# Performance work log

Hardware: AMD Instinct MI355X
Metric: run time of the kernel (lower is better)

The kernel has to match this reference:

```python
import jax, jax.numpy as jnp
import numpy as np

N_NODES = 100000
N_EDGES = 1600000
N_GRAPHS = 2048
F_IN = 33
D = 256


def _graph_conv(x, edge_index, w_rel, b_rel, w_root):
    # PyG GraphConv (aggr='add'): out = lin_rel(sum_j x_j) + lin_root(x)
    src, dst = edge_index[0], edge_index[1]
    agg = jax.ops.segment_sum(x[src], dst, num_segments=x.shape[0])  # [N, F]
    return agg @ w_rel + b_rel + x @ w_root


def setup_inputs() -> dict:
    key = jax.random.key(0)
    ks = jax.random.split(key, 16)
    scale_in = 1.0 / np.sqrt(F_IN)
    scale_d = 1.0 / np.sqrt(D)
    inp = {
        "x": jax.random.normal(ks[0], (N_NODES, F_IN), dtype=jnp.float32),
        "edge_index": jax.random.randint(ks[1], (2, N_EDGES), 0, N_NODES),
        "batch_index": jnp.sort(jax.random.randint(ks[2], (N_NODES,), 0, N_GRAPHS)),
        # initial_conv: GraphConv(F_IN -> D)
        "w_rel0": jax.random.normal(ks[3], (F_IN, D), dtype=jnp.float32) * scale_in,
        "b_rel0": jnp.zeros((D,), dtype=jnp.float32),
        "w_root0": jax.random.normal(ks[4], (F_IN, D), dtype=jnp.float32) * scale_in,
        # conv1..conv3: GraphConv(D -> D)
        "w_rel1": jax.random.normal(ks[5], (D, D), dtype=jnp.float32) * scale_d,
        "b_rel1": jnp.zeros((D,), dtype=jnp.float32),
        "w_root1": jax.random.normal(ks[6], (D, D), dtype=jnp.float32) * scale_d,
        "w_rel2": jax.random.normal(ks[7], (D, D), dtype=jnp.float32) * scale_d,
        "b_rel2": jnp.zeros((D,), dtype=jnp.float32),
        "w_root2": jax.random.normal(ks[8], (D, D), dtype=jnp.float32) * scale_d,
        "w_rel3": jax.random.normal(ks[9], (D, D), dtype=jnp.float32) * scale_d,
        "b_rel3": jnp.zeros((D,), dtype=jnp.float32),
        "w_root3": jax.random.normal(ks[10], (D, D), dtype=jnp.float32) * scale_d,
        # output head Linear(D -> 1)
        "w_out": jax.random.normal(ks[11], (D, 1), dtype=jnp.float32) * scale_d,
        "b_out": jnp.zeros((1,), dtype=jnp.float32),
    }
    return inp


def reference(x, edge_index, batch_index,
              w_rel0, b_rel0, w_root0,
              w_rel1, b_rel1, w_root1,
              w_rel2, b_rel2, w_root2,
              w_rel3, b_rel3, w_root3,
              w_out, b_out):
    # dropout omitted (eval mode)
    h = jax.nn.gelu(_graph_conv(x, edge_index, w_rel0, b_rel0, w_root0))
    h = jax.nn.gelu(_graph_conv(h, edge_index, w_rel1, b_rel1, w_root1))
    h = jax.nn.gelu(_graph_conv(h, edge_index, w_rel2, b_rel2, w_root2))
    h = jax.nn.gelu(_graph_conv(h, edge_index, w_rel3, b_rel3, w_root3))
    # global mean pool over graphs
    sums = jax.ops.segment_sum(h, batch_index, num_segments=N_GRAPHS)          # [G, D]
    counts = jax.ops.segment_sum(jnp.ones((h.shape[0],), h.dtype), batch_index,
                                 num_segments=N_GRAPHS)                         # [G]
    pooled = sums / jnp.maximum(counts, 1.0)[:, None]
    return pooled @ w_out + b_out                                               # [G, 1]
```

## Files before the change

### kernel.cpp

```cpp
#include <hip/hip_runtime.h>
#include <math.h>

#define NN 100000
#define NE 1600000
#define NG 2048
#define FIN 33
#define DD 256

#define SH 8
#define NB ((NN + 255) >> 8)
#define CH 4096
#define PCAP 4608
#define ESCAP 6144

#define RBLKS ((NN + 255) / 256)

typedef __attribute__((ext_vector_type(8))) short bf16x8;
typedef __attribute__((ext_vector_type(4))) float f32x4;

__device__ __forceinline__ float b2f(unsigned short u){
    union { unsigned int i; float f; } c; c.i = ((unsigned int)u) << 16; return c.f;
}
__device__ __forceinline__ unsigned short f2b(float f){
    union { float f; unsigned int u; } c; c.f = f;
    unsigned int r = c.u + 0x7fffu + ((c.u >> 16) & 1u);
    return (unsigned short)(r >> 16);
}

__device__ __forceinline__ float gelu_tanh(float x){
    float z = 0.7978845608028654f * (x + 0.044715f * x * x * x);
    return x / (1.0f + __expf(-2.0f * z));
}

__global__ __launch_bounds__(256) void k_bin(const int* __restrict__ src,
                                             const int* __restrict__ dst,
                                             int* __restrict__ gcur,
                                             int* __restrict__ pairs){
    __shared__ int cnt[NB];
    __shared__ int lb[NB];
    __shared__ int gbase[NB];
    __shared__ int sc[512];
    __shared__ int2 stage[CH];

    int t = threadIdx.x;
    for(int i = t; i < NB; i += 256) cnt[i] = 0;
    __syncthreads();

    int e0 = blockIdx.x * CH;
    int n = NE - e0; if(n > CH) n = CH;

    int  myb[16];
    int  myr[16];
    int2 myp[16];
    #pragma unroll
    for(int k = 0; k < 16; k++){
        int e = e0 + t + k * 256;
        if(e < NE){
            int s = src[e], d = dst[e];
            int b = d >> SH;
            myr[k] = atomicAdd(&cnt[b], 1);
            myb[k] = b;
            myp[k] = make_int2(s, d);
        } else myb[k] = -1;
    }
    __syncthreads();

    sc[t]       = (t       < NB) ? cnt[t]       : 0;
    sc[t + 256] = (t + 256 < NB) ? cnt[t + 256] : 0;
    __syncthreads();
    for(int off = 1; off < 512; off <<= 1){
        int a  = (t >= off)       ? sc[t - off]       : 0;
        int b2 = (t + 256 >= off) ? sc[t + 256 - off] : 0;
        __syncthreads();
        sc[t] += a; sc[t + 256] += b2;
        __syncthreads();
    }
    for(int i = t; i < NB; i += 256){
        lb[i] = sc[i] - cnt[i];
        int c = cnt[i];
        gbase[i] = (c > 0) ? atomicAdd(&gcur[i], c) : 0;
    }
    __syncthreads();

    #pragma unroll
    for(int k = 0; k < 16; k++){
        if(myb[k] >= 0) stage[lb[myb[k]] + myr[k]] = myp[k];
    }
    __syncthreads();

    for(int i = t; i < n; i += 256){
        int2 p = stage[i];
        int b = p.y >> SH;
        int tgt = gbase[b] + (i - lb[b]);
        if(tgt < PCAP) pairs[(size_t)b * PCAP + tgt] = p.x | ((p.y & 255) << 17);
    }
}

__global__ void k_sscan(const int* __restrict__ gcur, int* __restrict__ boff){
    __shared__ int s[512];
    int t = threadIdx.x;
    int v = 0;
    if(t < NB){ v = gcur[t]; if(v > PCAP) v = PCAP; }
    s[t] = v; __syncthreads();
    for(int off = 1; off < 512; off <<= 1){
        int u = (t >= off) ? s[t - off] : 0;
        __syncthreads();
        s[t] += u;
        __syncthreads();
    }
    if(t < NB) boff[t] = s[t] - v;
}

__global__ __launch_bounds__(256) void k_bcsr(const int* __restrict__ pairs,
                                              const int* __restrict__ gcur,
                                              const int* __restrict__ boff,
                                              int* __restrict__ deg,
                                              int* __restrict__ rs,
                                              int* __restrict__ esrc){
    __shared__ int hist[256];
    __shared__ int sc[256];
    __shared__ int cur2[256];
    __shared__ int est[ESCAP];

    int b = blockIdx.x;
    int t = threadIdx.x;
    int m = gcur[b]; if(m > PCAP) m = PCAP;
    int pstart = boff[b];
    const int* bp = pairs + (size_t)b * PCAP;

    hist[t] = 0;
    __syncthreads();
    for(int i = t; i < m; i += 256) atomicAdd(&hist[(bp[i] >> 17) & 255], 1);
    __syncthreads();

    sc[t] = hist[t]; __syncthreads();
    for(int off = 1; off < 256; off <<= 1){
        int u = (t >= off) ? sc[t - off] : 0;
        __syncthreads();
        sc[t] += u;
        __syncthreads();
    }
    int excl = sc[t] - hist[t];
    cur2[t] = excl;
    int node = (b << 8) + t;
    if(node < NN){
        deg[node] = hist[t];
        rs[node]  = pstart + excl;
    }
    __syncthreads();

    for(int i = t; i < m; i += 256){
        int p = bp[i];
        int pos = atomicAdd(&cur2[(p >> 17) & 255], 1);
        int s = p & 0x1FFFF;
        if(pos < ESCAP) est[pos] = s;
        else esrc[pstart + pos] = s;
    }
    __syncthreads();
    int lim = (m < ESCAP) ? m : ESCAP;
    for(int i = t; i < lim; i += 256) esrc[pstart + i] = est[i];
}

__global__ void k_xpad(const float* __restrict__ x, unsigned short* __restrict__ xb){
    int idx = blockIdx.x * 256 + threadIdx.x;
    if(idx >= NN * 64) return;
    int n = idx >> 6, c = idx & 63;
    xb[idx] = (c < FIN) ? f2b(x[(size_t)n * FIN + c]) : 0;
}

__global__ void k_aggx(const unsigned short* __restrict__ xb, const int* __restrict__ rs,
                       const int* __restrict__ deg, const int* __restrict__ esrc,
                       unsigned short* __restrict__ axb){
    int wv = (blockIdx.x * blockDim.x + threadIdx.x) >> 6;
    int lane = threadIdx.x & 63;
    int node = wv * 4 + (lane >> 4);
    int l16 = lane & 15;
    if(node >= NN) return;
    int start = rs[node], cnt = deg[node];
    float a0 = 0.f, a1 = 0.f, a2 = 0.f, a3 = 0.f;
    const unsigned short* xp = xb + l16 * 4;
    int j = 0;
    for(; j + 4 <= cnt; j += 4){
        int e0 = esrc[start+j], e1 = esrc[start+j+1], e2 = esrc[start+j+2], e3 = esrc[start+j+3];
        ushort4 v0 = *(const ushort4*)(xp + (size_t)e0 * 64);
        ushort4 v1 = *(const ushort4*)(xp + (size_t)e1 * 64);
        ushort4 v2 = *(const ushort4*)(xp + (size_t)e2 * 64);
        ushort4 v3 = *(const ushort4*)(xp + (size_t)e3 * 64);
        a0 += (b2f(v0.x) + b2f(v1.x)) + (b2f(v2.x) + b2f(v3.x));
        a1 += (b2f(v0.y) + b2f(v1.y)) + (b2f(v2.y) + b2f(v3.y));
        a2 += (b2f(v0.z) + b2f(v1.z)) + (b2f(v2.z) + b2f(v3.z));
        a3 += (b2f(v0.w) + b2f(v1.w)) + (b2f(v2.w) + b2f(v3.w));
    }
    for(; j < cnt; j++){
        int e = esrc[start + j];
        ushort4 v = *(const ushort4*)(xp + (size_t)e * 64);
        a0 += b2f(v.x); a1 += b2f(v.y); a2 += b2f(v.z); a3 += b2f(v.w);
    }
    ushort4 o; o.x = f2b(a0); o.y = f2b(a1); o.z = f2b(a2); o.w = f2b(a3);
    *(ushort4*)(axb + (size_t)node * 64 + l16 * 4) = o;
}

__global__ void k_agg256(const unsigned short* __restrict__ h, const int* __restrict__ rs,
                         const int* __restrict__ deg, const int* __restrict__ esrc,
                         unsigned short* __restrict__ agg){
    int wv = (blockIdx.x * blockDim.x + threadIdx.x) >> 6;
    int lane = threadIdx.x & 63;
    int node = wv * 2 + (lane >> 5);
    int l32 = lane & 31;
    if(node >= NN) return;
    int start = rs[node], cnt = deg[node];
    float a[8] = {0.f,0.f,0.f,0.f,0.f,0.f,0.f,0.f};
    const unsigned short* hp = h + l32 * 8;
    int j = 0;
    for(; j + 8 <= cnt; j += 8){
        bf16x8 v[8];
        #pragma unroll
        for(int q = 0; q < 8; q++){
            int e = esrc[start + j + q];
            v[q] = *(const bf16x8*)(hp + (size_t)e * DD);
        }
        #pragma unroll
        for(int q = 0; q < 8; q++)
            #pragma unroll
            for(int d = 0; d < 8; d++)
                a[d] += b2f((unsigned short)v[q][d]);
    }
    for(; j < cnt; j++){
        int e = esrc[start + j];
        bf16x8 v = *(const bf16x8*)(hp + (size_t)e * DD);
        #pragma unroll
        for(int d = 0; d < 8; d++) a[d] += b2f((unsigned short)v[d]);
    }
    bf16x8 o;
    #pragma unroll
    for(int d = 0; d < 8; d++) o[d] = (short)f2b(a[d]);
    *(bf16x8*)(agg + (size_t)node * DD + l32 * 8) = o;
}

struct WPtrs { const float* w[6]; };

__global__ void k_wt6(WPtrs wp, unsigned short* __restrict__ btAll){
    __shared__ float s[16][17];
    const float* W = wp.w[blockIdx.z];
    unsigned short* Bt = btAll + (size_t)blockIdx.z * DD * DD;
    int tx = threadIdx.x, ty = threadIdx.y;
    int k = blockIdx.y * 16 + ty;
    int j = blockIdx.x * 16 + tx;
    s[ty][tx] = W[k * DD + j];
    __syncthreads();
    Bt[(size_t)(blockIdx.x * 16 + ty) * DD + blockIdx.y * 16 + tx] = f2b(s[tx][ty]);
}

struct W2Ptrs { const float* w[2]; };

__global__ void k_wt0(W2Ptrs wp, unsigned short* __restrict__ btAll){
    int idx = blockIdx.x * 256 + threadIdx.x;
    if(idx >= DD * 64) return;
    const float* W = wp.w[blockIdx.z];
    unsigned short* Bt = btAll + (size_t)blockIdx.z * DD * 64;
    int j = idx >> 6, k = idx & 63;
    Bt[idx] = (k < FIN) ? f2b(W[(size_t)k * DD + j]) : 0;
}

__global__ void k_cnt(const int* __restrict__ batch, int* __restrict__ gcnt){
    int i = blockIdx.x * 256 + threadIdx.x;
    if(i < NN) atomicAdd(&gcnt[batch[i]], 1);
}

template<int KS, int AST, bool POOL>
__global__ __launch_bounds__(512, 4) void k_mfma_gemm(
    const unsigned short* __restrict__ A0, const unsigned short* __restrict__ A1,
    const unsigned short* __restrict__ Bt0, const unsigned short* __restrict__ Bt1,
    const float* __restrict__ bias, unsigned short* __restrict__ out,
    const int* __restrict__ batch, const float* __restrict__ wout,
    float* __restrict__ gsum)
{
    constexpr int CK  = KS * 32;
    constexpr int BST = CK + 8;
    constexpr int SEG = CK / 8;
    __shared__ unsigned short Bs[128 * BST];

    int t = threadIdx.x;
    int lane = t & 63;
    int w = t >> 6;
    int r16 = lane & 15;
    int kg  = lane >> 4;

    int bid = blockIdx.x;
    int rblk = (bid >> 4) * 8 + (bid & 7);
    int chalf = (bid >> 3) & 1;
    if(rblk >= RBLKS) return;
    int i0 = rblk * 256;
    int jbase = chalf * 128;
    int baseRow = i0 + w * 32;

    f32x4 acc[2][8];
    #pragma unroll
    for(int m = 0; m < 2; m++)
        #pragma unroll
        for(int n = 0; n < 8; n++)
            acc[m][n] = (f32x4){0.f, 0.f, 0.f, 0.f};

    auto loadA = [&](int gks, bf16x8* af){
        const unsigned short* Ap = (gks < KS) ? A0 : A1;
        int kk = ((gks < KS) ? gks : gks - KS) * 32 + kg * 8;
        #pragma unroll
        for(int m = 0; m < 2; m++){
            int gi = baseRow + m * 16 + r16;
            if(gi > NN - 1) gi = NN - 1;
            af[m] = *(const bf16x8*)(Ap + (size_t)gi * AST + kk);
        }
    };

    bf16x8 afb[2][2];
    loadA(0, afb[0]);
    loadA(1, afb[1]);

    #pragma unroll
    for(int c = 0; c < 2; c++){
        const unsigned short* Bp = c ? Bt1 : Bt0;
        if(c) __syncthreads();
        #pragma unroll
        for(int p = 0; p < (128 * SEG) / 512; p++){
            int idx = p * 512 + t;
            int row = idx / SEG;
            int k8 = (idx % SEG) * 8;
            *(bf16x8*)(&Bs[row * BST + k8]) =
                *(const bf16x8*)(Bp + (size_t)(jbase + row) * AST + k8);
        }
        __syncthreads();
        #pragma unroll
        for(int ksl = 0; ksl < KS; ksl++){
            int gks = c * KS + ksl;
            #pragma unroll
            for(int n = 0; n < 8; n++){
                bf16x8 bfr = *(const bf16x8*)(&Bs[(n * 16 + r16) * BST + ksl * 32 + kg * 8]);
                acc[0][n] = __builtin_amdgcn_mfma_f32_16x16x32_bf16(afb[gks & 1][0], bfr, acc[0][n], 0, 0, 0);
                acc[1][n] = __builtin_amdgcn_mfma_f32_16x16x32_bf16(afb[gks & 1][1], bfr, acc[1][n], 0, 0, 0);
            }
            if(gks + 2 < 2 * KS) loadA(gks + 2, afb[gks & 1]);
        }
    }

    int rg = kg * 4;
    if constexpr (!POOL){
        #pragma unroll
        for(int n = 0; n < 8; n++){
            int gj = jbase + n * 16 + r16;
            float bb = bias[gj];
            #pragma unroll
            for(int m = 0; m < 2; m++){
                #pragma unroll
                for(int r = 0; r < 4; r++){
                    int gi = baseRow + m * 16 + rg + r;
                    if(gi < NN)
                        out[(size_t)gi * DD + gj] = f2b(gelu_tanh(acc[m][n][r] + bb));
                }
            }
        }
    } else {
        #pragma unroll
        for(int m = 0; m < 2; m++){
            #pragma unroll
            for(int r = 0; r < 4; r++){
                float s = 0.f;
                #pragma unroll
                for(int n = 0; n < 8; n++){
                    int gj = jbase + n * 16 + r16;
                    s += gelu_tanh(acc[m][n][r] + bias[gj]) * wout[gj];
                }
                s += __shfl_xor(s, 1);
                s += __shfl_xor(s, 2);
                s += __shfl_xor(s, 4);
                s += __shfl_xor(s, 8);
                int gi = baseRow + m * 16 + rg + r;
                if(r16 == 0 && gi < NN)
                    atomicAdd(&gsum[batch[gi]], s);
            }
        }
    }
}

__global__ void k_final(const float* __restrict__ gsum, const int* __restrict__ gcnt,
                        const float* __restrict__ bout, float* __restrict__ out){
    int g = blockIdx.x * 256 + threadIdx.x;
    if(g < NG) out[g] = gsum[g] / fmaxf((float)gcnt[g], 1.f) + bout[0];
}

extern "C" void kernel_launch(void* const* d_in, const int* in_sizes, int n_in,
                              void* d_out, int out_size, void* d_ws, size_t ws_size,
                              hipStream_t stream){
    const float* x       = (const float*)d_in[0];
    const int*   ei      = (const int*)d_in[1];
    const int*   src     = ei;
    const int*   dst     = ei + NE;
    const int*   batch   = (const int*)d_in[2];
    const float* w_rel0  = (const float*)d_in[3];
    const float* b_rel0  = (const float*)d_in[4];
    const float* w_root0 = (const float*)d_in[5];
    const float* w_rel1  = (const float*)d_in[6];
    const float* b_rel1  = (const float*)d_in[7];
    const float* w_root1 = (const float*)d_in[8];
    const float* w_rel2  = (const float*)d_in[9];
    const float* b_rel2  = (const float*)d_in[10];
    const float* w_root2 = (const float*)d_in[11];
    const float* w_rel3  = (const float*)d_in[12];
    const float* b_rel3  = (const float*)d_in[13];
    const float* w_root3 = (const float*)d_in[14];
    const float* w_out   = (const float*)d_in[15];
    const float* b_out   = (const float*)d_in[16];
    float* out = (float*)d_out;

    char* ws = (char*)d_ws;
    size_t off = 0;
    auto alloc = [&](size_t bytes) -> void* {
        void* p = ws + off;
        off = (off + bytes + 255) & ~(size_t)255;
        return p;
    };
    unsigned short* hA  = (unsigned short*)alloc((size_t)NN * DD * 2);
    unsigned short* hB  = (unsigned short*)alloc((size_t)NN * DD * 2);
    unsigned short* agg = (unsigned short*)alloc((size_t)NN * DD * 2);
    int*   deg  = (int*)alloc((size_t)NN * 4);
    int*   rs   = (int*)alloc((size_t)NN * 4);
    int*   esrc = (int*)alloc((size_t)NE * 4);
    int*   gcur = (int*)alloc(512 * 4);
    int*   boff = (int*)alloc(512 * 4);
    float* gsum = (float*)alloc((size_t)NG * 4);
    int*   gcnt = (int*)alloc((size_t)NG * 4);
    unsigned short* btAll = (unsigned short*)alloc((size_t)6 * DD * DD * 2);
    unsigned short* bt0All = (unsigned short*)alloc((size_t)2 * DD * 64 * 2);
    (void)ws_size; (void)in_sizes; (void)n_in; (void)out_size;

    int* pairs = (int*)hB;
    unsigned short* xb  = agg;
    unsigned short* axb = agg + (size_t)NN * 64 + 128;

    hipMemsetAsync(gcur, 0, 512 * 4, stream);
    k_bin<<<(NE + CH - 1) / CH, 256, 0, stream>>>(src, dst, gcur, pairs);
    k_sscan<<<1, 512, 0, stream>>>(gcur, boff);
    k_bcsr<<<NB, 256, 0, stream>>>(pairs, gcur, boff, deg, rs, esrc);

    size_t poolBytes = (size_t)((char*)(gcnt + NG) - (char*)gsum);
    hipMemsetAsync(gsum, 0, poolBytes, stream);
    k_cnt<<<(NN + 255) / 256, 256, 0, stream>>>(batch, gcnt);

    WPtrs wp; wp.w[0] = w_rel1; wp.w[1] = w_root1; wp.w[2] = w_rel2;
    wp.w[3] = w_root2; wp.w[4] = w_rel3; wp.w[5] = w_root3;
    k_wt6<<<dim3(16, 16, 6), dim3(16, 16), 0, stream>>>(wp, btAll);
    W2Ptrs w2; w2.w[0] = w_rel0; w2.w[1] = w_root0;
    k_wt0<<<dim3((DD * 64 + 255) / 256, 1, 2), 256, 0, stream>>>(w2, bt0All);
    k_xpad<<<(NN * 64 + 255) / 256, 256, 0, stream>>>(x, xb);

    unsigned short* bt[6];
    for(int i = 0; i < 6; i++) bt[i] = btAll + (size_t)i * DD * DD;
    unsigned short* bt0r = bt0All;
    unsigned short* bt0o = bt0All + (size_t)DD * 64;

    int agg2Grid = (NN * 32 + 255) / 256;
    int gemmGrid = ((RBLKS + 7) / 8) * 16;

    k_aggx<<<(NN + 15) / 16, 256, 0, stream>>>(xb, rs, deg, esrc, axb);
    k_mfma_gemm<2, 64, false><<<gemmGrid, 512, 0, stream>>>(axb, xb, bt0r, bt0o, b_rel0, hA,
                                                            batch, w_out, gsum);
    k_agg256<<<agg2Grid, 256, 0, stream>>>(hA, rs, deg, esrc, agg);
    k_mfma_gemm<8, 256, false><<<gemmGrid, 512, 0, stream>>>(agg, hA, bt[0], bt[1], b_rel1, hB,
                                                             batch, w_out, gsum);
    k_agg256<<<agg2Grid, 256, 0, stream>>>(hB, rs, deg, esrc, agg);
    k_mfma_gemm<8, 256, false><<<gemmGrid, 512, 0, stream>>>(agg, hB, bt[2], bt[3], b_rel2, hA,
                                                             batch, w_out, gsum);
    k_agg256<<<agg2Grid, 256, 0, stream>>>(hA, rs, deg, esrc, agg);
    k_mfma_gemm<8, 256, true><<<gemmGrid, 512, 0, stream>>>(agg, hA, bt[4], bt[5], b_rel3, hB,
                                                            batch, w_out, gsum);

    k_final<<<(NG + 255) / 256, 256, 0, stream>>>(gsum, gcnt, b_out, out);
}
```

Baseline: 739.7 us.

## Pre-swizzle weights into MFMA fragment layout and drop LDS staging in GEMM

Adds a k_bfrag pre-pass that rearranges the transposed bf16 weights into per-lane MFMA fragment order. The GEMM then reads B fragments straight from global memory (expected to hit L2) with coalesced 16-byte loads, so the LDS tile and its __syncthreads barriers are gone. Blocks shrink to 256 threads and 128 rows, which doubles the grid. The A prefetch double-buffering is also removed, so A loads are no longer overlapped with MFMA and global-memory latency is exposed on every k-step.

```diff
diff --git a/kernel.cpp b/kernel.cpp
--- a/kernel.cpp
+++ b/kernel.cpp
@@ -13,7 +13,7 @@
 #define PCAP 4608
 #define ESCAP 6144
 
-#define RBLKS ((NN + 255) / 256)
+#define RB128 ((NN + 127) / 128)
 
 typedef __attribute__((ext_vector_type(8))) short bf16x8;
 typedef __attribute__((ext_vector_type(4))) float f32x4;
@@ -262,24 +262,34 @@
     Bt[idx] = (k < FIN) ? f2b(W[(size_t)k * DD + j]) : 0;
 }
 
+__global__ void k_bfrag(const unsigned short* __restrict__ btBase,
+                        unsigned short* __restrict__ bfBase,
+                        int ast, int nslots, int inStride, int outStride){
+    int slot = blockIdx.x * 256 + threadIdx.x;
+    if(slot >= nslots) return;
+    const unsigned short* Bt = btBase + (size_t)blockIdx.z * inStride;
+    unsigned short* bf = bfBase + (size_t)blockIdx.z * outStride;
+    int ks = slot >> 10;
+    int rem = slot & 1023;
+    int n = rem >> 6;
+    int l = rem & 63;
+    bf16x8 v = *(const bf16x8*)(Bt + (size_t)(n * 16 + (l & 15)) * ast + ks * 32 + (l >> 4) * 8);
+    *(bf16x8*)(bf + (size_t)slot * 8) = v;
+}
+
 __global__ void k_cnt(const int* __restrict__ batch, int* __restrict__ gcnt){
     int i = blockIdx.x * 256 + threadIdx.x;
     if(i < NN) atomicAdd(&gcnt[batch[i]], 1);
 }
 
 template<int KS, int AST, bool POOL>
-__global__ __launch_bounds__(512, 4) void k_mfma_gemm(
+__global__ __launch_bounds__(256, 4) void k_gemm_nl(
     const unsigned short* __restrict__ A0, const unsigned short* __restrict__ A1,
-    const unsigned short* __restrict__ Bt0, const unsigned short* __restrict__ Bt1,
+    const unsigned short* __restrict__ bp0, const unsigned short* __restrict__ bp1,
     const float* __restrict__ bias, unsigned short* __restrict__ out,
     const int* __restrict__ batch, const float* __restrict__ wout,
     float* __restrict__ gsum)
 {
-    constexpr int CK  = KS * 32;
-    constexpr int BST = CK + 8;
-    constexpr int SEG = CK / 8;
-    __shared__ unsigned short Bs[128 * BST];
-
     int t = threadIdx.x;
     int lane = t & 63;
     int w = t >> 6;
@@ -289,8 +299,8 @@
     int bid = blockIdx.x;
     int rblk = (bid >> 4) * 8 + (bid & 7);
     int chalf = (bid >> 3) & 1;
-    if(rblk >= RBLKS) return;
-    int i0 = rblk * 256;
+    if(rblk >= RB128) return;
+    int i0 = rblk * 128;
     int jbase = chalf * 128;
     int baseRow = i0 + w * 32;
 
@@ -301,44 +311,27 @@
         for(int n = 0; n < 8; n++)
             acc[m][n] = (f32x4){0.f, 0.f, 0.f, 0.f};
 
-    auto loadA = [&](int gks, bf16x8* af){
-        const unsigned short* Ap = (gks < KS) ? A0 : A1;
-        int kk = ((gks < KS) ? gks : gks - KS) * 32 + kg * 8;
-        #pragma unroll
-        for(int m = 0; m < 2; m++){
-            int gi = baseRow + m * 16 + r16;
-            if(gi > NN - 1) gi = NN - 1;
-            af[m] = *(const bf16x8*)(Ap + (size_t)gi * AST + kk);
-        }
-    };
-
-    bf16x8 afb[2][2];
-    loadA(0, afb[0]);
-    loadA(1, afb[1]);
-
     #pragma unroll
     for(int c = 0; c < 2; c++){
-        const unsigned short* Bp = c ? Bt1 : Bt0;
-        if(c) __syncthreads();
-        #pragma unroll
-        for(int p = 0; p < (128 * SEG) / 512; p++){
-            int idx = p * 512 + t;
-            int row = idx / SEG;
-            int k8 = (idx % SEG) * 8;
-            *(bf16x8*)(&Bs[row * BST + k8]) =
-                *(const bf16x8*)(Bp + (size_t)(jbase + row) * AST + k8);
-        }
-        __syncthreads();
+        const unsigned short* Ap = c ? A1 : A0;
+        const unsigned short* Bp = c ? bp1 : bp0;
         #pragma unroll
         for(int ksl = 0; ksl < KS; ksl++){
-            int gks = c * KS + ksl;
+            int kk = ksl * 32 + kg * 8;
+            bf16x8 af[2];
+            #pragma unroll
+            for(int m = 0; m < 2; m++){
+                int gi = baseRow + m * 16 + r16;
+                if(gi > NN - 1) gi = NN - 1;
+                af[m] = *(const bf16x8*)(Ap + (size_t)gi * AST + kk);
+            }
+            const unsigned short* bpp = Bp + (size_t)((ksl * 16 + chalf * 8) * 64 + lane) * 8;
             #pragma unroll
             for(int n = 0; n < 8; n++){
-                bf16x8 bfr = *(const bf16x8*)(&Bs[(n * 16 + r16) * BST + ksl * 32 + kg * 8]);
-                acc[0][n] = __builtin_amdgcn_mfma_f32_16x16x32_bf16(afb[gks & 1][0], bfr, acc[0][n], 0, 0, 0);
-                acc[1][n] = __builtin_amdgcn_mfma_f32_16x16x32_bf16(afb[gks & 1][1], bfr, acc[1][n], 0, 0, 0);
+                bf16x8 bfr = *(const bf16x8*)(bpp + (size_t)n * 64 * 8);
+                acc[0][n] = __builtin_amdgcn_mfma_f32_16x16x32_bf16(af[0], bfr, acc[0][n], 0, 0, 0);
+                acc[1][n] = __builtin_amdgcn_mfma_f32_16x16x32_bf16(af[1], bfr, acc[1][n], 0, 0, 0);
             }
-            if(gks + 2 < 2 * KS) loadA(gks + 2, afb[gks & 1]);
         }
     }
 
@@ -428,8 +421,10 @@
     int*   boff = (int*)alloc(512 * 4);
     float* gsum = (float*)alloc((size_t)NG * 4);
     int*   gcnt = (int*)alloc((size_t)NG * 4);
-    unsigned short* btAll = (unsigned short*)alloc((size_t)6 * DD * DD * 2);
+    unsigned short* btAll  = (unsigned short*)alloc((size_t)6 * DD * DD * 2);
     unsigned short* bt0All = (unsigned short*)alloc((size_t)2 * DD * 64 * 2);
+    unsigned short* bfAll  = (unsigned short*)alloc((size_t)6 * DD * DD * 2);
+    unsigned short* bf0All = (unsigned short*)alloc((size_t)2 * DD * 64 * 2);
     (void)ws_size; (void)in_sizes; (void)n_in; (void)out_size;
 
     int* pairs = (int*)hB;
@@ -452,26 +447,29 @@
     k_wt0<<<dim3((DD * 64 + 255) / 256, 1, 2), 256, 0, stream>>>(w2, bt0All);
     k_xpad<<<(NN * 64 + 255) / 256, 256, 0, stream>>>(x, xb);
 
-    unsigned short* bt[6];
-    for(int i = 0; i < 6; i++) bt[i] = btAll + (size_t)i * DD * DD;
-    unsigned short* bt0r = bt0All;
-    unsigned short* bt0o = bt0All + (size_t)DD * 64;
+    k_bfrag<<<dim3(8192 / 256, 1, 6), 256, 0, stream>>>(btAll, bfAll, DD, 8192, DD * DD, DD * DD);
+    k_bfrag<<<dim3(2048 / 256, 1, 2), 256, 0, stream>>>(bt0All, bf0All, 64, 2048, DD * 64, DD * 64);
+
+    unsigned short* bf[6];
+    for(int i = 0; i < 6; i++) bf[i] = bfAll + (size_t)i * DD * DD;
+    unsigned short* bf0r = bf0All;
+    unsigned short* bf0o = bf0All + (size_t)DD * 64;
 
     int agg2Grid = (NN * 32 + 255) / 256;
-    int gemmGrid = ((RBLKS + 7) / 8) * 16;
+    int gemmGrid = ((RB128 + 7) / 8) * 16;
 
     k_aggx<<<(NN + 15) / 16, 256, 0, stream>>>(xb, rs, deg, esrc, axb);
-    k_mfma_gemm<2, 64, false><<<gemmGrid, 512, 0, stream>>>(axb, xb, bt0r, bt0o, b_rel0, hA,
-                                                            batch, w_out, gsum);
+    k_gemm_nl<2, 64, false><<<gemmGrid, 256, 0, stream>>>(axb, xb, bf0r, bf0o, b_rel0, hA,
+                                                          batch, w_out, gsum);
     k_agg256<<<agg2Grid, 256, 0, stream>>>(hA, rs, deg, esrc, agg);
-    k_mfma_gemm<8, 256, false><<<gemmGrid, 512, 0, stream>>>(agg, hA, bt[0], bt[1], b_rel1, hB,
-                                                             batch, w_out, gsum);
+    k_gemm_nl<8, 256, false><<<gemmGrid, 256, 0, stream>>>(agg, hA, bf[0], bf[1], b_rel1, hB,
+                                                           batch, w_out, gsum);
     k_agg256<<<agg2Grid, 256, 0, stream>>>(hB, rs, deg, esrc, agg);
-    k_mfma_gemm<8, 256, false><<<gemmGrid, 512, 0, stream>>>(agg, hB, bt[2], bt[3], b_rel2, hA,
-                                                             batch, w_out, gsum);
+    k_gemm_nl<8, 256, false><<<gemmGrid, 256, 0, stream>>>(agg, hB, bf[2], bf[3], b_rel2, hA,
+                                                           batch, w_out, gsum);
     k_agg256<<<agg2Grid, 256, 0, stream>>>(hA, rs, deg, esrc, agg);
-    k_mfma_gemm<8, 256, true><<<gemmGrid, 512, 0, stream>>>(agg, hA, bt[4], bt[5], b_rel3, hB,
-                                                            batch, w_out, gsum);
+    k_gemm_nl<8, 256, true><<<gemmGrid, 256, 0, stream>>>(agg, hA, bf[4], bf[5], b_rel3, hB,
+                                                          batch, w_out, gsum);
 
     k_final<<<(NG + 255) / 256, 256, 0, stream>>>(gsum, gcnt, b_out, out);
 }
```

After: 830.1 us. +12.2%, slower.

## Overlap root-term GEMM with neighbor aggregation in a heterogeneous kernel

Applied to the files above, without the earlier changes.

Replaces the aggregation kernel with a heterogeneous kernel. Eight of every nine blocks gather neighbor sums, and the ninth computes the root GEMM (h @ W_root + bias) into a scratch buffer, using B fragments pre-arranged in MFMA lane order so they load directly from global memory. The following GEMM then does only the rel half and adds the stored root result before GELU, writing in place over that buffer. The aim is to overlap memory-bound gathers with compute-bound MFMA work, at the cost of an extra bf16 round-trip for the root partial (adding rounding error) and a root GEMM that runs without LDS reuse.

```diff
diff --git a/kernel.cpp b/kernel.cpp
--- a/kernel.cpp
+++ b/kernel.cpp
@@ -14,6 +14,8 @@
 #define ESCAP 6144
 
 #define RBLKS ((NN + 255) / 256)
+#define RB128 ((NN + 127) / 128)
+#define NGRP  (RB128 * 2)
 
 typedef __attribute__((ext_vector_type(8))) short bf16x8;
 typedef __attribute__((ext_vector_type(4))) float f32x4;
@@ -200,43 +202,6 @@
     *(ushort4*)(axb + (size_t)node * 64 + l16 * 4) = o;
 }
 
-__global__ void k_agg256(const unsigned short* __restrict__ h, const int* __restrict__ rs,
-                         const int* __restrict__ deg, const int* __restrict__ esrc,
-                         unsigned short* __restrict__ agg){
-    int wv = (blockIdx.x * blockDim.x + threadIdx.x) >> 6;
-    int lane = threadIdx.x & 63;
-    int node = wv * 2 + (lane >> 5);
-    int l32 = lane & 31;
-    if(node >= NN) return;
-    int start = rs[node], cnt = deg[node];
-    float a[8] = {0.f,0.f,0.f,0.f,0.f,0.f,0.f,0.f};
-    const unsigned short* hp = h + l32 * 8;
-    int j = 0;
-    for(; j + 8 <= cnt; j += 8){
-        bf16x8 v[8];
-        #pragma unroll
-        for(int q = 0; q < 8; q++){
-            int e = esrc[start + j + q];
-            v[q] = *(const bf16x8*)(hp + (size_t)e * DD);
-        }
-        #pragma unroll
-        for(int q = 0; q < 8; q++)
-            #pragma unroll
-            for(int d = 0; d < 8; d++)
-                a[d] += b2f((unsigned short)v[q][d]);
-    }
-    for(; j < cnt; j++){
-        int e = esrc[start + j];
-        bf16x8 v = *(const bf16x8*)(hp + (size_t)e * DD);
-        #pragma unroll
-        for(int d = 0; d < 8; d++) a[d] += b2f((unsigned short)v[d]);
-    }
-    bf16x8 o;
-    #pragma unroll
-    for(int d = 0; d < 8; d++) o[d] = (short)f2b(a[d]);
-    *(bf16x8*)(agg + (size_t)node * DD + l32 * 8) = o;
-}
-
 struct WPtrs { const float* w[6]; };
 
 __global__ void k_wt6(WPtrs wp, unsigned short* __restrict__ btAll){
@@ -262,22 +227,132 @@
     Bt[idx] = (k < FIN) ? f2b(W[(size_t)k * DD + j]) : 0;
 }
 
+__global__ void k_bfrag(const unsigned short* __restrict__ Bt,
+                        unsigned short* __restrict__ bf){
+    int slot = blockIdx.x * 256 + threadIdx.x;
+    if(slot >= 8192) return;
+    int ks = slot >> 10;
+    int rem = slot & 1023;
+    int n = rem >> 6;
+    int l = rem & 63;
+    bf16x8 v = *(const bf16x8*)(Bt + (size_t)(n * 16 + (l & 15)) * DD + ks * 32 + (l >> 4) * 8);
+    *(bf16x8*)(bf + (size_t)slot * 8) = v;
+}
+
 __global__ void k_cnt(const int* __restrict__ batch, int* __restrict__ gcnt){
     int i = blockIdx.x * 256 + threadIdx.x;
     if(i < NN) atomicAdd(&gcnt[batch[i]], 1);
 }
 
-template<int KS, int AST, bool POOL>
-__global__ __launch_bounds__(512, 4) void k_mfma_gemm(
+__global__ __launch_bounds__(256) void k_het2(
+    const unsigned short* __restrict__ h,
+    const int* __restrict__ rs, const int* __restrict__ deg, const int* __restrict__ esrc,
+    unsigned short* __restrict__ agg,
+    const unsigned short* __restrict__ bfRoot,
+    const float* __restrict__ bias,
+    unsigned short* __restrict__ R)
+{
+    int bid = blockIdx.x;
+    int q = bid / 9, rr = bid % 9;
+    int t = threadIdx.x;
+    int lane = t & 63;
+    int w = t >> 6;
+
+    if(rr < 8){
+        int node = (q * 8 + rr) * 8 + w * 2 + (lane >> 5);
+        int l32 = lane & 31;
+        if(node >= NN) return;
+        int start = rs[node], cnt = deg[node];
+        float a[8] = {0.f,0.f,0.f,0.f,0.f,0.f,0.f,0.f};
+        const unsigned short* hp = h + l32 * 8;
+        int j = 0;
+        for(; j + 8 <= cnt; j += 8){
+            bf16x8 v[8];
+            #pragma unroll
+            for(int qq = 0; qq < 8; qq++){
+                int e = esrc[start + j + qq];
+                v[qq] = *(const bf16x8*)(hp + (size_t)e * DD);
+            }
+            #pragma unroll
+            for(int qq = 0; qq < 8; qq++)
+                #pragma unroll
+                for(int d = 0; d < 8; d++)
+                    a[d] += b2f((unsigned short)v[qq][d]);
+        }
+        for(; j < cnt; j++){
+            int e = esrc[start + j];
+            bf16x8 v = *(const bf16x8*)(hp + (size_t)e * DD);
+            #pragma unroll
+            for(int d = 0; d < 8; d++) a[d] += b2f((unsigned short)v[d]);
+        }
+        bf16x8 o;
+        #pragma unroll
+        for(int d = 0; d < 8; d++) o[d] = (short)f2b(a[d]);
+        *(bf16x8*)(agg + (size_t)node * DD + l32 * 8) = o;
+    } else {
+        int rblk = q >> 1, chalf = q & 1;
+        int i0 = rblk * 128;
+        int jbase = chalf * 128;
+        int r16 = lane & 15, kg = lane >> 4;
+        int baseRow = i0 + w * 32;
+
+        f32x4 acc[2][8];
+        #pragma unroll
+        for(int m = 0; m < 2; m++)
+            #pragma unroll
+            for(int n = 0; n < 8; n++)
+                acc[m][n] = (f32x4){0.f, 0.f, 0.f, 0.f};
+
+        #pragma unroll
+        for(int ksl = 0; ksl < 8; ksl++){
+            int kk = ksl * 32 + kg * 8;
+            bf16x8 af[2];
+            #pragma unroll
+            for(int m = 0; m < 2; m++){
+                int gi = baseRow + m * 16 + r16;
+                if(gi > NN - 1) gi = NN - 1;
+                af[m] = *(const bf16x8*)(h + (size_t)gi * DD + kk);
+            }
+            const unsigned short* bpp = bfRoot + (size_t)((ksl * 16 + chalf * 8) * 64 + lane) * 8;
+            #pragma unroll
+            for(int n = 0; n < 8; n++){
+                bf16x8 bfr = *(const bf16x8*)(bpp + (size_t)n * 64 * 8);
+                acc[0][n] = __builtin_amdgcn_mfma_f32_16x16x32_bf16(af[0], bfr, acc[0][n], 0, 0, 0);
+                acc[1][n] = __builtin_amdgcn_mfma_f32_16x16x32_bf16(af[1], bfr, acc[1][n], 0, 0, 0);
+            }
+        }
+
+        int rg = kg * 4;
+        #pragma unroll
+        for(int n = 0; n < 8; n++){
+            int gj = jbase + n * 16 + r16;
+            float bb = bias[gj];
+            #pragma unroll
+            for(int m = 0; m < 2; m++){
+                #pragma unroll
+                for(int r = 0; r < 4; r++){
+                    int gi = baseRow + m * 16 + rg + r;
+                    if(gi < NN)
+                        R[(size_t)gi * DD + gj] = f2b(acc[m][n][r] + bb);
+                }
+            }
+        }
+    }
+}
+
+template<int KS, int AST, bool DUAL, bool POOL>
+__global__ __launch_bounds__(512, 4) void k_gemm(
     const unsigned short* __restrict__ A0, const unsigned short* __restrict__ A1,
     const unsigned short* __restrict__ Bt0, const unsigned short* __restrict__ Bt1,
     const float* __restrict__ bias, unsigned short* __restrict__ out,
+    unsigned short* __restrict__ R,
     const int* __restrict__ batch, const float* __restrict__ wout,
     float* __restrict__ gsum)
 {
     constexpr int CK  = KS * 32;
     constexpr int BST = CK + 8;
     constexpr int SEG = CK / 8;
+    constexpr int NMAT = DUAL ? 2 : 1;
     __shared__ unsigned short Bs[128 * BST];
 
     int t = threadIdx.x;
@@ -317,7 +392,7 @@
     loadA(1, afb[1]);
 
     #pragma unroll
-    for(int c = 0; c < 2; c++){
+    for(int c = 0; c < NMAT; c++){
         const unsigned short* Bp = c ? Bt1 : Bt0;
         if(c) __syncthreads();
         #pragma unroll
@@ -338,7 +413,7 @@
                 acc[0][n] = __builtin_amdgcn_mfma_f32_16x16x32_bf16(afb[gks & 1][0], bfr, acc[0][n], 0, 0, 0);
                 acc[1][n] = __builtin_amdgcn_mfma_f32_16x16x32_bf16(afb[gks & 1][1], bfr, acc[1][n], 0, 0, 0);
             }
-            if(gks + 2 < 2 * KS) loadA(gks + 2, afb[gks & 1]);
+            if(gks + 2 < NMAT * KS) loadA(gks + 2, afb[gks & 1]);
         }
     }
 
@@ -347,14 +422,17 @@
         #pragma unroll
         for(int n = 0; n < 8; n++){
             int gj = jbase + n * 16 + r16;
-            float bb = bias[gj];
+            float bb = DUAL ? bias[gj] : 0.f;
             #pragma unroll
             for(int m = 0; m < 2; m++){
                 #pragma unroll
                 for(int r = 0; r < 4; r++){
                     int gi = baseRow + m * 16 + rg + r;
-                    if(gi < NN)
-                        out[(size_t)gi * DD + gj] = f2b(gelu_tanh(acc[m][n][r] + bb));
+                    if(gi < NN){
+                        size_t adr = (size_t)gi * DD + gj;
+                        float v = acc[m][n][r] + (DUAL ? bb : b2f(R[adr]));
+                        out[adr] = f2b(gelu_tanh(v));
+                    }
                 }
             }
         }
@@ -363,17 +441,18 @@
         for(int m = 0; m < 2; m++){
             #pragma unroll
             for(int r = 0; r < 4; r++){
+                int gi = baseRow + m * 16 + rg + r;
                 float s = 0.f;
                 #pragma unroll
                 for(int n = 0; n < 8; n++){
                     int gj = jbase + n * 16 + r16;
-                    s += gelu_tanh(acc[m][n][r] + bias[gj]) * wout[gj];
+                    float rv = (gi < NN) ? b2f(R[(size_t)gi * DD + gj]) : 0.f;
+                    s += gelu_tanh(acc[m][n][r] + rv) * wout[gj];
                 }
                 s += __shfl_xor(s, 1);
                 s += __shfl_xor(s, 2);
                 s += __shfl_xor(s, 4);
                 s += __shfl_xor(s, 8);
-                int gi = baseRow + m * 16 + rg + r;
                 if(r16 == 0 && gi < NN)
                     atomicAdd(&gsum[batch[gi]], s);
             }
@@ -428,8 +507,9 @@
     int*   boff = (int*)alloc(512 * 4);
     float* gsum = (float*)alloc((size_t)NG * 4);
     int*   gcnt = (int*)alloc((size_t)NG * 4);
-    unsigned short* btAll = (unsigned short*)alloc((size_t)6 * DD * DD * 2);
+    unsigned short* btAll  = (unsigned short*)alloc((size_t)6 * DD * DD * 2);
     unsigned short* bt0All = (unsigned short*)alloc((size_t)2 * DD * 64 * 2);
+    unsigned short* bfRoot = (unsigned short*)alloc((size_t)3 * DD * DD * 2);
     (void)ws_size; (void)in_sizes; (void)n_in; (void)out_size;
 
     int* pairs = (int*)hB;
@@ -456,22 +536,28 @@
     for(int i = 0; i < 6; i++) bt[i] = btAll + (size_t)i * DD * DD;
     unsigned short* bt0r = bt0All;
     unsigned short* bt0o = bt0All + (size_t)DD * 64;
-
-    int agg2Grid = (NN * 32 + 255) / 256;
+    unsigned short* bfr1 = bfRoot;
+    unsigned short* bfr2 = bfRoot + (size_t)DD * DD;
+    unsigned short* bfr3 = bfRoot + (size_t)2 * DD * DD;
+    k_bfrag<<<32, 256, 0, stream>>>(bt[1], bfr1);
+    k_bfrag<<<32, 256, 0, stream>>>(bt[3], bfr2);
+    k_bfrag<<<32, 256, 0, stream>>>(bt[5], bfr3);
+
+    int hetGrid  = NGRP * 9;
     int gemmGrid = ((RBLKS + 7) / 8) * 16;
 
     k_aggx<<<(NN + 15) / 16, 256, 0, stream>>>(xb, rs, deg, esrc, axb);
-    k_mfma_gemm<2, 64, false><<<gemmGrid, 512, 0, stream>>>(axb, xb, bt0r, bt0o, b_rel0, hA,
-                                                            batch, w_out, gsum);
-    k_agg256<<<agg2Grid, 256, 0, stream>>>(hA, rs, deg, esrc, agg);
-    k_mfma_gemm<8, 256, false><<<gemmGrid, 512, 0, stream>>>(agg, hA, bt[0], bt[1], b_rel1, hB,
-                                                             batch, w_out, gsum);
-    k_agg256<<<agg2Grid, 256, 0, stream>>>(hB, rs, deg, esrc, agg);
-    k_mfma_gemm<8, 256, false><<<gemmGrid, 512, 0, stream>>>(agg, hB, bt[2], bt[3], b_rel2, hA,
-                                                             batch, w_out, gsum);
-    k_agg256<<<agg2Grid, 256, 0, stream>>>(hA, rs, deg, esrc, agg);
-    k_mfma_gemm<8, 256, true><<<gemmGrid, 512, 0, stream>>>(agg, hA, bt[4], bt[5], b_rel3, hB,
-                                                            batch, w_out, gsum);
+    k_gemm<2, 64, true, false><<<gemmGrid, 512, 0, stream>>>(axb, xb, bt0r, bt0o, b_rel0, hA,
+                                                             nullptr, batch, w_out, gsum);
+    k_het2<<<hetGrid, 256, 0, stream>>>(hA, rs, deg, esrc, agg, bfr1, b_rel1, hB);
+    k_gemm<8, 256, false, false><<<gemmGrid, 512, 0, stream>>>(agg, nullptr, bt[0], nullptr,
+                                                               nullptr, hB, hB, batch, w_out, gsum);
+    k_het2<<<hetGrid, 256, 0, stream>>>(hB, rs, deg, esrc, agg, bfr2, b_rel2, hA);
+    k_gemm<8, 256, false, false><<<gemmGrid, 512, 0, stream>>>(agg, nullptr, bt[2], nullptr,
+                                                               nullptr, hA, hA, batch, w_out, gsum);
+    k_het2<<<hetGrid, 256, 0, stream>>>(hA, rs, deg, esrc, agg, bfr3, b_rel3, hB);
+    k_gemm<8, 256, false, true><<<gemmGrid, 512, 0, stream>>>(agg, nullptr, bt[4], nullptr,
+                                                              nullptr, hB, hB, batch, w_out, gsum);
 
     k_final<<<(NG + 255) / 256, 256, 0, stream>>>(gsum, gcnt, b_out, out);
 }
```

Measured after the change: 1.124 ms. 1.52x slower.
